# Optimization experiments

Measured on AMD Instinct MI355X. Metric: run time of the kernel, lower is better.

The kernel has to match this reference:

```python
import math
import jax, jax.numpy as jnp
import numpy as np

H = 256      # hidden_size
HEADS = 8
DK = H // HEADS
B = 32
DL = 290     # drug length
PL = 1000    # protein length


def _pe(length, d):
    # sinusoidal positional encoding, d even
    pos = jnp.arange(length, dtype=jnp.float32)[:, None]
    div = jnp.exp(jnp.arange(0, d, 2, dtype=jnp.float32) * (-math.log(10000.0) / d))
    ang = pos * div  # [L, d/2]
    pe = jnp.zeros((length, d), jnp.float32)
    pe = pe.at[:, 0::2].set(jnp.sin(ang)).at[:, 1::2].set(jnp.cos(ang))
    return pe


def setup_inputs() -> dict:
    key = jax.random.key(0)
    ks = iter(jax.random.split(key, 48))
    def lin(din, dout):
        return jax.random.normal(next(ks), (din, dout), jnp.float32) * 0.02, jnp.zeros((dout,), jnp.float32)
    inp = {}
    inp['drug'] = jax.random.normal(next(ks), (B, DL, H), jnp.float32)
    inp['protein'] = jax.random.normal(next(ks), (B, PL, H), jnp.float32)
    inp['scale_d'] = jnp.ones((1,), jnp.float32)
    inp['scale_p'] = jnp.ones((1,), jnp.float32)
    for name in ['q_d', 'k_p', 'v_p', 'q_p', 'k_d', 'v_d', 'out_d', 'out_p']:
        w, b = lin(H, H)
        inp['w_' + name] = w
        inp['b_' + name] = b
    inp['alpha'] = jnp.asarray(0.5, jnp.float32)
    for name in ['fc_dp', 'fc_pd']:
        w, b = lin(HEADS, H)
        inp['w_' + name] = w
        inp['b_' + name] = b
    for name in ['gd', 'gp']:
        w, b = lin(H, H)
        inp['w_' + name] = w
        inp['b_' + name] = b
    return inp


def _split_heads(x):
    b, l, _ = x.shape
    return x.reshape(b, l, HEADS, DK).transpose(0, 2, 1, 3)  # [b, h, l, dk]


def _forward(drug, protein, scale_d, scale_p,
             w_q_d, b_q_d, w_k_p, b_k_p, w_v_p, b_v_p,
             w_q_p, b_q_p, w_k_d, b_k_d, w_v_d, b_v_d,
             alpha, w_out_d, b_out_d, w_out_p, b_out_p,
             w_fc_dp, b_fc_dp, w_fc_pd, b_fc_pd,
             w_gd, b_gd, w_gp, b_gp):
    b, dl, h = drug.shape
    pl = protein.shape[1]
    # positional encoding (buffers, non-learned except scale)
    drug_e = drug + scale_d * _pe(dl, h)
    prot_e = protein + scale_p * _pe(pl, h)

    Qd = _split_heads(drug_e @ w_q_d + b_q_d)   # [b,h,dl,dk]
    Kp = _split_heads(prot_e @ w_k_p + b_k_p)   # [b,h,pl,dk]
    Vp = _split_heads(prot_e @ w_v_p + b_v_p)
    Qp = _split_heads(prot_e @ w_q_p + b_q_p)
    Kd = _split_heads(drug_e @ w_k_d + b_k_d)
    Vd = _split_heads(drug_e @ w_v_d + b_v_d)

    inv_sqrt = 1.0 / math.sqrt(DK)
    attn_dp = jnp.einsum('bhid,bhjd->bhij', Qd, Kp) * inv_sqrt      # [b,h,dl,pl]
    # (Q_p K_d^T)^T along last two dims -> [b,h,dl,pl]
    attn_pd = jnp.einsum('bhjd,bhid->bhij', Qp, Kd) * inv_sqrt
    a = jax.nn.sigmoid(alpha)
    A = jax.nn.softmax(a * attn_dp + (1.0 - a) * attn_pd, axis=-1)  # [b,h,dl,pl]

    ctx_d = jnp.einsum('bhij,bhjd->bhid', A, Vp)  # [b,h,dl,dk]
    ctx_p = jnp.einsum('bhij,bhid->bhjd', A, Vd)  # [b,h,pl,dk]
    ctx_d = ctx_d.transpose(0, 2, 1, 3).reshape(b, dl, h) @ w_out_d + b_out_d
    ctx_p = ctx_p.transpose(0, 2, 1, 3).reshape(b, pl, h) @ w_out_p + b_out_p

    attn_dp_m = jnp.mean(A, axis=-1).transpose(0, 2, 1)   # [b,dl,heads]
    drug_attn = attn_dp_m @ w_fc_dp + b_fc_dp             # [b,dl,h]
    attn_pd_m = jnp.mean(A, axis=-2).transpose(0, 2, 1)   # [b,pl,heads]
    prot_attn = attn_pd_m @ w_fc_pd + b_fc_pd             # [b,pl,h]

    drug_gate = jax.nn.sigmoid(drug_e @ w_gd + b_gd)
    prot_gate = jax.nn.sigmoid(prot_e @ w_gp + b_gp)
    ctx_d = ctx_d * drug_gate
    ctx_p = ctx_p * prot_gate

    drug_upd = drug_e + ctx_d * jax.nn.sigmoid(drug_attn)
    prot_upd = prot_e + ctx_p * jax.nn.sigmoid(prot_attn)
    return jnp.concatenate([drug_upd, prot_upd], axis=1)  # [b, dl+pl, h]


def reference(drug, protein, scale_d, scale_p,
              w_q_d, b_q_d, w_k_p, b_k_p, w_v_p, b_v_p,
              w_q_p, b_q_p, w_k_d, b_k_d, w_v_d, b_v_d,
              alpha, w_out_d, b_out_d, w_out_p, b_out_p,
              w_fc_dp, b_fc_dp, w_fc_pd, b_fc_pd,
              w_gd, b_gd, w_gp, b_gp):
    return _forward(drug, protein, scale_d, scale_p,
                    w_q_d, b_q_d, w_k_p, b_k_p, w_v_p, b_v_p,
                    w_q_p, b_q_p, w_k_d, b_k_d, w_v_d, b_v_d,
                    alpha, w_out_d, b_out_d, w_out_p, b_out_p,
                    w_fc_dp, b_fc_dp, w_fc_pd, b_fc_pd,
                    w_gd, b_gd, w_gp, b_gp)
```

## Files before the change

kernel.cpp:

```cpp
#include <hip/hip_runtime.h>
#include <math.h>

typedef __attribute__((ext_vector_type(8))) short bf16x8;
typedef __attribute__((ext_vector_type(4))) float f32x4;
typedef unsigned short u16;
typedef unsigned int u32;

#define DEVFN static __device__ __forceinline__

constexpr int NB  = 32;
constexpr int DLn = 290;
constexpr int PLc = 1000;
constexpr int MD  = NB * DLn;
constexpr int MP  = NB * PLc;
constexpr int NSTRIP = 645;
constexpr int SPLIT  = 145;
constexpr int SG     = 81;

DEVFN u16 f2b(float f) {
    u32 u = __builtin_bit_cast(u32, f);
    u32 r = u + 0x7fffu + ((u >> 16) & 1u);
    return (u16)(r >> 16);
}
DEVFN u16 f2bh(float f) { __bf16 h = (__bf16)f; return __builtin_bit_cast(u16, h); }
DEVFN float b2f(u16 s) { return __builtin_bit_cast(float, (u32)s << 16); }
DEVFN float sigm(float x) { return 1.0f / (1.0f + __expf(-x)); }
DEVFN float fexp2(float x) { return __builtin_amdgcn_exp2f(x); }
DEVFN int sw(int row, int col, int stride) { return row * stride + (col ^ ((row & 7) << 3)); }

__global__ void pe_kernel(float* __restrict__ pe) {
    int p = blockIdx.x, c = threadIdx.x;
    float div = __expf((float)(c & ~1) * (-9.210340371976184f / 256.0f));
    float ang = (float)p * div;
    pe[p * 256 + c] = (c & 1) ? cosf(ang) : sinf(ang);
}

__global__ void fcprep_kernel(const float* __restrict__ w, const float* __restrict__ b,
                              float* __restrict__ dfc) {
    int c = threadIdx.x;
    float s = b[c];
    #pragma unroll
    for (int hh = 0; hh < 8; hh++) s += 0.001f * w[hh * 256 + c];
    dfc[c] = s;
}

__global__ __launch_bounds__(256) void eadd_kernel(
        const float* __restrict__ drug, const float* __restrict__ prot,
        const float* __restrict__ scale_d, const float* __restrict__ scale_p,
        const float* __restrict__ pe,
        u16* __restrict__ e_d, u16* __restrict__ e_p) {
    int idx = blockIdx.x * 256 + threadIdx.x;
    int r = idx >> 6, c4 = (idx & 63) * 4;
    if (r < MD) {
        int i = r % DLn;
        float s = scale_d[0];
        float4 dv = *(const float4*)&drug[(size_t)r * 256 + c4];
        float4 pv = *(const float4*)&pe[i * 256 + c4];
        u16 o[4];
        o[0] = f2b(dv.x + s * pv.x); o[1] = f2b(dv.y + s * pv.y);
        o[2] = f2b(dv.z + s * pv.z); o[3] = f2b(dv.w + s * pv.w);
        *(uint2*)&e_d[(size_t)r * 256 + c4] = *(uint2*)o;
    } else {
        int rr = r - MD;
        int j = rr % PLc;
        float s = scale_p[0];
        float4 dv = *(const float4*)&prot[(size_t)rr * 256 + c4];
        float4 pv = *(const float4*)&pe[j * 256 + c4];
        u16 o[4];
        o[0] = f2b(dv.x + s * pv.x); o[1] = f2b(dv.y + s * pv.y);
        o[2] = f2b(dv.z + s * pv.z); o[3] = f2b(dv.w + s * pv.w);
        *(uint2*)&e_p[(size_t)rr * 256 + c4] = *(uint2*)o;
    }
}

struct WPtrs { const float* w[10]; };
__global__ __launch_bounds__(256) void wprep_kernel(WPtrs wp, u16* __restrict__ wt) {
    __shared__ u16 t[64][66];
    int m = blockIdx.y, tile = blockIdx.x;
    int k0 = (tile >> 2) * 64, n0 = (tile & 3) * 64;
    const float* w = wp.w[m];
    int r = threadIdx.x >> 6, c = threadIdx.x & 63;
    #pragma unroll
    for (int q = 0; q < 16; q++) {
        int rr = r + q * 4;
        t[rr][c] = f2b(w[(size_t)(k0 + rr) * 256 + n0 + c]);
    }
    __syncthreads();
    #pragma unroll
    for (int q = 0; q < 16; q++) {
        int rr = r + q * 4;
        wt[((size_t)m << 16) + (size_t)(n0 + rr) * 256 + k0 + c] = t[c][rr];
    }
}

struct PM { const u16* BT; const float* bias; u16* C; int sig; };
struct PCfg {
    const u16* Ab;
    PM m[4];
};
struct PCfg2 {
    PCfg c0, c1;
    const float* x0; const float* x1;
    const u16* gate0; const u16* gate1;
    const float* cm;
    const float* dfc;
    const float* wfc1; const float* bfc1;
    const float* scale0; const float* scale1;
    const float* pe;
    float* out;
};

template<int NM>
__global__ __launch_bounds__(256) void proj_kernel(PCfg2 cfgs) {
    const int d = blockIdx.x;
    const int x = d & 7, q = d >> 3;
    const int u  = (NM == 4) ? (q & 15) : (q & 3);
    const int sg = (NM == 4) ? (q >> 4) : (q >> 2);
    const int s = sg * 8 + x;
    if (s >= NSTRIP) return;
    const int mi = (NM == 4) ? (u >> 2) : 0;
    const int nt = (NM == 4) ? (u & 3) : u;
    const bool f1 = s < SPLIT;
    const int mt = f1 ? s : s - SPLIT;

    const u16* Ab   = f1 ? cfgs.c0.Ab : cfgs.c1.Ab;
    const u16*   BT   = f1 ? (mi==0?cfgs.c0.m[0].BT  :mi==1?cfgs.c0.m[1].BT  :mi==2?cfgs.c0.m[2].BT  :cfgs.c0.m[3].BT)
                           : (mi==0?cfgs.c1.m[0].BT  :mi==1?cfgs.c1.m[1].BT  :mi==2?cfgs.c1.m[2].BT  :cfgs.c1.m[3].BT);
    const float* bias = f1 ? (mi==0?cfgs.c0.m[0].bias:mi==1?cfgs.c0.m[1].bias:mi==2?cfgs.c0.m[2].bias:cfgs.c0.m[3].bias)
                           : (mi==0?cfgs.c1.m[0].bias:mi==1?cfgs.c1.m[1].bias:mi==2?cfgs.c1.m[2].bias:cfgs.c1.m[3].bias);
    u16*         C    = f1 ? (mi==0?cfgs.c0.m[0].C   :mi==1?cfgs.c0.m[1].C   :mi==2?cfgs.c0.m[2].C   :cfgs.c0.m[3].C)
                           : (mi==0?cfgs.c1.m[0].C   :mi==1?cfgs.c1.m[1].C   :mi==2?cfgs.c1.m[2].C   :cfgs.c1.m[3].C);
    const int    sig  = f1 ? (mi==0?cfgs.c0.m[0].sig :mi==1?cfgs.c0.m[1].sig :mi==2?cfgs.c0.m[2].sig :cfgs.c0.m[3].sig)
                           : (mi==0?cfgs.c1.m[0].sig :mi==1?cfgs.c1.m[1].sig :mi==2?cfgs.c1.m[2].sig :cfgs.c1.m[3].sig);

    __shared__ u16 Bs[64 * 256];
    __shared__ float fcb[(NM == 1) ? 2304 : 4];
    const int tid = threadIdx.x;
    const int lane = tid & 63, w = tid >> 6, ln = lane & 15, g = lane >> 4;

    const int gc = tid & 31;
    const int rb = (tid >> 5) * 8;
    uint4 bv[8];
    #pragma unroll
    for (int kk = 0; kk < 8; kk++) {
        const int r = rb + kk;
        const int nur = ((r >> 5) & 1) * 32 + ((r >> 2) & 3) * 8 + ((r >> 4) & 1) * 4 + (r & 3);
        bv[kk] = *(const uint4*)(BT + (size_t)(nt * 64 + nur) * 256 + gc * 8);
    }

    const int row = mt * 64 + w * 16 + ln;
    bf16x8 Af[8];
    {
        const u16* Ap = Ab + (size_t)row * 256 + g * 8;
        #pragma unroll
        for (int ks = 0; ks < 8; ks++)
            Af[ks] = *(const bf16x8*)(Ap + ks * 32);
    }

    if (NM == 1 && !f1) {
        *(float4*)&fcb[tid * 8]     = *(const float4*)&cfgs.wfc1[tid * 8];
        *(float4*)&fcb[tid * 8 + 4] = *(const float4*)&cfgs.wfc1[tid * 8 + 4];
        fcb[2048 + tid] = cfgs.bfc1[tid];
    }

    #pragma unroll
    for (int kk = 0; kk < 8; kk++) {
        const int r = rb + kk;
        *(uint4*)&Bs[sw(r, gc * 8, 256)] = bv[kk];
    }
    __syncthreads();

    f32x4 acc[4] = {};
    #pragma unroll
    for (int ks = 0; ks < 8; ks++) {
        #pragma unroll
        for (int ntl = 0; ntl < 4; ntl++) {
            bf16x8 bf = *(const bf16x8*)&Bs[sw(ntl * 16 + ln, ks * 32 + g * 8, 256)];
            acc[ntl] = __builtin_amdgcn_mfma_f32_16x16x32_bf16(bf, Af[ks], acc[ntl], 0, 0, 0);
        }
    }

    const int base0 = nt * 64 + g * 8, base1 = base0 + 32;
    f32x4 b0 = *(const f32x4*)&bias[base0];
    f32x4 b1 = *(const f32x4*)&bias[base0 + 4];
    f32x4 b2 = *(const f32x4*)&bias[base1];
    f32x4 b3 = *(const f32x4*)&bias[base1 + 4];
    float v[16];
    #pragma unroll
    for (int t = 0; t < 4; t++) {
        v[t]      = acc[0][t] + b0[t];
        v[4 + t]  = acc[1][t] + b1[t];
        v[8 + t]  = acc[2][t] + b2[t];
        v[12 + t] = acc[3][t] + b3[t];
    }
    if (NM == 4) {
        if (sig) {
            #pragma unroll
            for (int t = 0; t < 16; t++) v[t] = sigm(v[t]);
        }
        u16 o[16];
        #pragma unroll
        for (int t = 0; t < 16; t++) o[t] = f2b(v[t]);
        u16* Cp = C + (size_t)row * 256;
        *(uint4*)&Cp[base0] = *(uint4*)&o[0];
        *(uint4*)&Cp[base1] = *(uint4*)&o[8];
    } else {
        (void)C; (void)sig;
        const float* X     = f1 ? cfgs.x0 : cfgs.x1;
        const u16* gate    = f1 ? cfgs.gate0 : cfgs.gate1;
        const float* scale = f1 ? cfgs.scale0 : cfgs.scale1;
        const float* pe    = cfgs.pe;
        const float sc = scale[0];
        const int pos  = f1 ? (row % DLn) : (row % PLc);
        const int bidx = f1 ? (row / DLn) : (row / PLc);
        const int orow = bidx * 1290 + (f1 ? pos : 290 + pos);
        float aw[16];
        if (f1) {
            const float* dfc = cfgs.dfc;
            *(float4*)&aw[0]  = *(const float4*)&dfc[base0];
            *(float4*)&aw[4]  = *(const float4*)&dfc[base0 + 4];
            *(float4*)&aw[8]  = *(const float4*)&dfc[base1];
            *(float4*)&aw[12] = *(const float4*)&dfc[base1 + 4];
        } else {
            float cmv[8];
            float4 ca = *(const float4*)&cfgs.cm[(size_t)row * 8];
            float4 cb = *(const float4*)&cfgs.cm[(size_t)row * 8 + 4];
            cmv[0]=ca.x; cmv[1]=ca.y; cmv[2]=ca.z; cmv[3]=ca.w;
            cmv[4]=cb.x; cmv[5]=cb.y; cmv[6]=cb.z; cmv[7]=cb.w;
            #pragma unroll
            for (int t = 0; t < 16; t++) {
                const int col = (t < 8) ? (base0 + t) : (base1 + t - 8);
                float s2 = fcb[2048 + col];
                #pragma unroll
                for (int hh = 0; hh < 8; hh++) s2 += cmv[hh] * fcb[hh * 256 + col];
                aw[t] = s2;
            }
        }
        u16 ge[16];
        *(uint4*)&ge[0] = *(const uint4*)&gate[(size_t)row * 256 + base0];
        *(uint4*)&ge[8] = *(const uint4*)&gate[(size_t)row * 256 + base1];
        float outv[16];
        #pragma unroll
        for (int half = 0; half < 2; half++) {
            const int cb0 = half ? base1 : base0;
            #pragma unroll
            for (int t4 = 0; t4 < 2; t4++) {
                float4 xa = *(const float4*)&X[(size_t)row * 256 + cb0 + t4 * 4];
                float4 pa = *(const float4*)&pe[(size_t)pos * 256 + cb0 + t4 * 4];
                #pragma unroll
                for (int t = 0; t < 4; t++) {
                    const int idx = half * 8 + t4 * 4 + t;
                    float e = (&xa.x)[t] + sc * (&pa.x)[t];
                    outv[idx] = e + v[idx] * b2f(ge[idx]) * sigm(aw[idx]);
                }
            }
        }
        float* Op = cfgs.out + (size_t)orow * 256;
        *(float4*)&Op[base0]     = *(float4*)&outv[0];
        *(float4*)&Op[base0 + 4] = *(float4*)&outv[4];
        *(float4*)&Op[base1]     = *(float4*)&outv[8];
        *(float4*)&Op[base1 + 4] = *(float4*)&outv[12];
    }
}

__global__ __launch_bounds__(512) void attn_kernel(
        const u16* __restrict__ Qd, const u16* __restrict__ Kd, const u16* __restrict__ Vd,
        const u16* __restrict__ Kp, const u16* __restrict__ Vp, const u16* __restrict__ Qp,
        const float* __restrict__ alpha,
        u16* __restrict__ ctx_d, u16* __restrict__ ctx_p, float* __restrict__ cm) {
    __shared__ u16 Ks[2][64 * 64];
    __shared__ union {
        struct { u16 VpT[2][32 * 64]; u16 Pm[320 * 64]; } s1;
        struct { u16 PT[64 * 320]; u16 VdT[32 * 320]; } s2;
    } U;
    __shared__ float r_l[320];
    __shared__ float colpart[8][64];

    const int bh = blockIdx.x, b = bh >> 3, h = bh & 7;
    const int tid = threadIdx.x;
    const int w = tid >> 6, lane = tid & 63, ln = lane & 15, g = lane >> 4;

    const float a = sigm(alpha[0]);
    const float inv = 0.1767766952966369f;
    const float l2e = 1.4426950408889634f;
    const float sa = a * inv * l2e, sb = (1.0f - a) * inv * l2e;
    const int nmt = (w < 4) ? 3 : 2;
    const int mtsA[3] = { w, w + 8, w + 16 };

    const size_t rbd = (size_t)b * DLn * 256 + h * 32;
    const size_t rbp = (size_t)b * PLc * 256 + h * 32;

    bf16x8 Qf[3][2];
    #pragma unroll
    for (int t = 0; t < 3; t++) {
        const int i = mtsA[t] * 16 + ln;
        #pragma unroll
        for (int ks = 0; ks < 2; ks++) {
            u16 o[8] = {0,0,0,0,0,0,0,0};
            if (t < nmt && i < DLn) {
                const u16* src = (ks ? Kd : Qd) + rbd + (size_t)i * 256 + g * 8;
                const float s = ks ? sb : sa;
                uint4 v = *(const uint4*)src;
                u16 e[8]; *(uint4*)e = v;
                #pragma unroll
                for (int q = 0; q < 8; q++) o[q] = f2bh(b2f(e[q]) * s);
            }
            Qf[t][ks] = *(bf16x8*)o;
        }
    }

    const int s_jj = tid >> 3, s_ch = tid & 7;
    const u16* s_src = ((s_ch >> 2) ? Qp : Kp) + rbp + (s_ch & 3) * 8;
    const int v_j = tid & 63, v_d0 = (tid >> 6) * 4;

    {
        int j = s_jj;
        uint4 kv = (j < PLc) ? *(const uint4*)(s_src + (size_t)j * 256) : make_uint4(0,0,0,0);
        uint2 vv = (v_j < PLc) ? *(const uint2*)(Vp + rbp + (size_t)v_j * 256 + v_d0) : make_uint2(0,0);
        *(uint4*)&Ks[0][sw(s_jj, s_ch * 8, 64)] = kv;
        u16 e[4]; *(uint2*)e = vv;
        #pragma unroll
        for (int q = 0; q < 4; q++) U.s1.VpT[0][sw(v_d0 + q, v_j, 64)] = e[q];
    }
    __syncthreads();

    float rs[3] = {0.f, 0.f, 0.f};
    f32x4 accd[3][2] = {};
    for (int jt = 0; jt < 16; jt++) {
        const int cur = jt & 1, j0 = jt * 64;
        const int jn = j0 + 64 + s_jj;
        uint4 kv = (jn < PLc) ? *(const uint4*)(s_src + (size_t)jn * 256) : make_uint4(0,0,0,0);
        const int vn = j0 + 64 + v_j;
        uint2 vv = (vn < PLc) ? *(const uint2*)(Vp + rbp + (size_t)vn * 256 + v_d0) : make_uint2(0,0);

        bf16x8 kf[4][2];
        #pragma unroll
        for (int js = 0; js < 4; js++)
            #pragma unroll
            for (int ks = 0; ks < 2; ks++)
                kf[js][ks] = *(const bf16x8*)&Ks[cur][sw(js * 16 + ln, ks * 32 + g * 8, 64)];

        #pragma unroll
        for (int t = 0; t < 3; t++) {
            if (t >= nmt) break;
            const int mt = mtsA[t];
            f32x4 acc[4] = {};
            #pragma unroll
            for (int ks = 0; ks < 2; ks++)
                #pragma unroll
                for (int js = 0; js < 4; js++)
                    acc[js] = __builtin_amdgcn_mfma_f32_16x16x32_bf16(kf[js][ks], Qf[t][ks], acc[js], 0, 0, 0);
            const int irow = mt * 16 + ln;
            #pragma unroll
            for (int js = 0; js < 4; js++) {
                u16 pb[4];
                float psum = 0.f;
                #pragma unroll
                for (int r = 0; r < 4; r++) {
                    float p = fexp2(acc[js][r]);
                    psum += p;
                    pb[r] = f2bh(p);
                }
                rs[t] += psum;
                *(ushort4*)&U.s1.Pm[sw(irow, js * 16 + g * 4, 64)] = *(ushort4*)pb;
            }
        }
        #pragma unroll
        for (int t = 0; t < 3; t++) {
            if (t >= nmt) break;
            const int mt = mtsA[t];
            #pragma unroll
            for (int ks2 = 0; ks2 < 2; ks2++) {
                bf16x8 af = *(const bf16x8*)&U.s1.Pm[sw(mt * 16 + ln, ks2 * 32 + g * 8, 64)];
                #pragma unroll
                for (int nd = 0; nd < 2; nd++) {
                    bf16x8 bv = *(const bf16x8*)&U.s1.VpT[cur][sw(nd * 16 + ln, ks2 * 32 + g * 8, 64)];
                    accd[t][nd] = __builtin_amdgcn_mfma_f32_16x16x32_bf16(bv, af, accd[t][nd], 0, 0, 0);
                }
            }
        }
        *(uint4*)&Ks[cur ^ 1][sw(s_jj, s_ch * 8, 64)] = kv;
        {
            u16 e[4]; *(uint2*)e = vv;
            #pragma unroll
            for (int q = 0; q < 4; q++) U.s1.VpT[cur ^ 1][sw(v_d0 + q, v_j, 64)] = e[q];
        }
        __syncthreads();
    }

    #pragma unroll
    for (int t = 0; t < 3; t++) {
        float v = rs[t];
        v += __shfl_xor(v, 16);
        v += __shfl_xor(v, 32);
        rs[t] = v;
    }
    if (g == 0) {
        #pragma unroll
        for (int t = 0; t < 3; t++) {
            if (t >= nmt) break;
            const int i = mtsA[t] * 16 + ln;
            r_l[i] = (i < DLn) ? 1.0f / (rs[t] - 24.0f) : 0.0f;
        }
    }
    __syncthreads();

    #pragma unroll
    for (int t = 0; t < 3; t++) {
        if (t >= nmt) break;
        const int i = mtsA[t] * 16 + ln;
        if (i < DLn) {
            const float ri = r_l[i];
            #pragma unroll
            for (int nd = 0; nd < 2; nd++) {
                u16 o[4];
                #pragma unroll
                for (int r = 0; r < 4; r++) o[r] = f2bh(accd[t][nd][r] * ri);
                *(uint2*)&ctx_d[rbd + (size_t)i * 256 + nd * 16 + g * 4] = *(uint2*)o;
            }
        }
    }
    for (int c = tid; c < 320 * 8; c += 512) {
        const int i = c >> 3, d0 = (c & 7) * 4;
        u16 o[4] = {0,0,0,0};
        if (i < DLn) {
            const float ri = r_l[i];
            uint2 v = *(const uint2*)(Vd + rbd + (size_t)i * 256 + d0);
            u16 e[4]; *(uint2*)e = v;
            #pragma unroll
            for (int q = 0; q < 4; q++) o[q] = f2bh(b2f(e[q]) * ri);
        }
        #pragma unroll
        for (int q = 0; q < 4; q++) U.s2.VdT[sw(d0 + q, i, 320)] = o[q];
    }
    {
        int j = s_jj;
        uint4 kv = (j < PLc) ? *(const uint4*)(s_src + (size_t)j * 256) : make_uint4(0,0,0,0);
        *(uint4*)&Ks[0][sw(s_jj, s_ch * 8, 64)] = kv;
    }
    float rr[3][4];
    #pragma unroll
    for (int t = 0; t < 3; t++)
        #pragma unroll
        for (int r = 0; r < 4; r++)
            rr[t][r] = (t < nmt) ? r_l[mtsA[t] * 16 + g * 4 + r] : 0.0f;
    __syncthreads();

    for (int jt = 0; jt < 16; jt++) {
        const int cur = jt & 1, j0 = jt * 64;
        const int jn = j0 + 64 + s_jj;
        uint4 kv = (jn < PLc) ? *(const uint4*)(s_src + (size_t)jn * 256) : make_uint4(0,0,0,0);

        bf16x8 kf[4][2];
        #pragma unroll
        for (int js = 0; js < 4; js++)
            #pragma unroll
            for (int ks = 0; ks < 2; ks++)
                kf[js][ks] = *(const bf16x8*)&Ks[cur][sw(js * 16 + ln, ks * 32 + g * 8, 64)];

        float csl[4] = {0.f, 0.f, 0.f, 0.f};
        #pragma unroll
        for (int t = 0; t < 3; t++) {
            if (t >= nmt) break;
            const int mt = mtsA[t];
            f32x4 acc[4] = {};
            #pragma unroll
            for (int ks = 0; ks < 2; ks++)
                #pragma unroll
                for (int js = 0; js < 4; js++)
                    acc[js] = __builtin_amdgcn_mfma_f32_16x16x32_bf16(Qf[t][ks], kf[js][ks], acc[js], 0, 0, 0);
            #pragma unroll
            for (int js = 0; js < 4; js++) {
                u16 pb[4];
                #pragma unroll
                for (int r = 0; r < 4; r++) {
                    float p = fexp2(acc[js][r]);
                    csl[js] += p * rr[t][r];
                    pb[r] = f2bh(p);
                }
                *(ushort4*)&U.s2.PT[sw(js * 16 + ln, mt * 16 + g * 4, 320)] = *(ushort4*)pb;
            }
        }
        #pragma unroll
        for (int js = 0; js < 4; js++) {
            float v = csl[js];
            v += __shfl_xor(v, 16);
            v += __shfl_xor(v, 32);
            csl[js] = v;
        }
        if (g == 0) {
            #pragma unroll
            for (int js = 0; js < 4; js++) colpart[w][js * 16 + ln] = csl[js];
        }
        *(uint4*)&Ks[cur ^ 1][sw(s_jj, s_ch * 8, 64)] = kv;
        __syncthreads();

        {
            const int js2 = w & 3, ds2 = w >> 2;
            f32x4 ap = {};
            #pragma unroll
            for (int k = 0; k < 10; k++) {
                bf16x8 af = *(const bf16x8*)&U.s2.PT[sw(js2 * 16 + ln, k * 32 + g * 8, 320)];
                bf16x8 bv = *(const bf16x8*)&U.s2.VdT[sw(ds2 * 16 + ln, k * 32 + g * 8, 320)];
                ap = __builtin_amdgcn_mfma_f32_16x16x32_bf16(bv, af, ap, 0, 0, 0);
            }
            const int j = j0 + js2 * 16 + ln;
            if (j < PLc) {
                u16 o[4];
                #pragma unroll
                for (int r = 0; r < 4; r++) o[r] = f2bh(ap[r]);
                *(uint2*)&ctx_p[rbp + (size_t)j * 256 + ds2 * 16 + g * 4] = *(uint2*)o;
            }
        }
        if (w == 0) {
            float tot = 0.f;
            #pragma unroll
            for (int ww = 0; ww < 8; ww++) tot += colpart[ww][lane];
            const int j = j0 + lane;
            if (j < PLc) cm[(size_t)(b * PLc + j) * 8 + h] = tot * (1.0f / 290.0f);
        }
        __syncthreads();
    }
}

extern "C" void kernel_launch(void* const* d_in, const int* in_sizes, int n_in,
                              void* d_out, int out_size, void* d_ws, size_t ws_size,
                              hipStream_t stream) {
    (void)in_sizes; (void)n_in; (void)out_size;
    const float* drug    = (const float*)d_in[0];
    const float* prot    = (const float*)d_in[1];
    const float* scale_d = (const float*)d_in[2];
    const float* scale_p = (const float*)d_in[3];

    char* ws = (char*)d_ws;
    size_t off = 0;
    auto alloc = [&](size_t bytes) -> void* {
        void* p = ws + off;
        off += (bytes + 255) & ~(size_t)255;
        return p;
    };
    float* pe   = (float*)alloc((size_t)1000 * 256 * 4);
    u16* wt     = (u16*)alloc((size_t)10 * 65536 * 2);
    u16* e_d    = (u16*)alloc((size_t)MD * 256 * 2);
    u16* e_p    = (u16*)alloc((size_t)MP * 256 * 2);
    u16* Qd     = (u16*)alloc((size_t)MD * 256 * 2);
    u16* Kd     = (u16*)alloc((size_t)MD * 256 * 2);
    u16* Vd     = (u16*)alloc((size_t)MD * 256 * 2);
    u16* gate_d = (u16*)alloc((size_t)MD * 256 * 2);
    u16* Kp     = (u16*)alloc((size_t)MP * 256 * 2);
    u16* Vp     = (u16*)alloc((size_t)MP * 256 * 2);
    u16* Qp     = (u16*)alloc((size_t)MP * 256 * 2);
    u16* gate_p = (u16*)alloc((size_t)MP * 256 * 2);
    u16* ctxd   = (u16*)alloc((size_t)MD * 256 * 2);
    u16* ctxp   = (u16*)alloc((size_t)MP * 256 * 2);
    float* cm   = (float*)alloc((size_t)MP * 8 * 4);
    float* dfc  = (float*)alloc((size_t)256 * 4);
    if (off > ws_size) return;

    pe_kernel<<<1000, 256, 0, stream>>>(pe);
    fcprep_kernel<<<1, 256, 0, stream>>>((const float*)d_in[21], (const float*)d_in[22], dfc);

    WPtrs wp;
    const int wsrc[10] = {4, 12, 14, 25, 6, 8, 10, 27, 16, 18};
    for (int m = 0; m < 10; m++) wp.w[m] = (const float*)d_in[wsrc[m]];
    wprep_kernel<<<dim3(16, 10), 256, 0, stream>>>(wp, wt);

    eadd_kernel<<<(MD + MP) / 4, 256, 0, stream>>>(drug, prot, scale_d, scale_p, pe, e_d, e_p);

    auto W = [&](int slot) { return wt + (size_t)slot * 65536; };

    PCfg2 p1 = {};
    p1.c0 = { e_d,
              { { W(0), (const float*)d_in[5],  Qd,     0 },
                { W(1), (const float*)d_in[13], Kd,     0 },
                { W(2), (const float*)d_in[15], Vd,     0 },
                { W(3), (const float*)d_in[26], gate_d, 1 } } };
    p1.c1 = { e_p,
              { { W(4), (const float*)d_in[7],  Kp,     0 },
                { W(5), (const float*)d_in[9],  Vp,     0 },
                { W(6), (const float*)d_in[11], Qp,     0 },
                { W(7), (const float*)d_in[28], gate_p, 1 } } };
    proj_kernel<4><<<SG * 8 * 16, 256, 0, stream>>>(p1);

    attn_kernel<<<256, 512, 0, stream>>>(Qd, Kd, Vd, Kp, Vp, Qp,
                                         (const float*)d_in[20], ctxd, ctxp, cm);

    PCfg2 p2 = {};
    p2.c0 = { ctxd, { { W(8), (const float*)d_in[17], nullptr, 0 }, {}, {}, {} } };
    p2.c1 = { ctxp, { { W(9), (const float*)d_in[19], nullptr, 0 }, {}, {}, {} } };
    p2.x0 = drug;  p2.x1 = prot;
    p2.gate0 = gate_d;  p2.gate1 = gate_p;
    p2.cm = cm;
    p2.dfc = dfc;
    p2.wfc1 = (const float*)d_in[23];  p2.bfc1 = (const float*)d_in[24];
    p2.scale0 = scale_d;  p2.scale1 = scale_p;
    p2.pe = pe;
    p2.out = (float*)d_out;
    proj_kernel<1><<<SG * 8 * 4, 256, 0, stream>>>(p2);
}
```

Measured before the change: 175.3 us.

## Split attention over drug-row halves to double block count, merge partials downstream

The attention kernel now runs two blocks per (batch, head), each handling half of the drug rows (160 padded). Each half writes its own partial protein-side context and column-mean buffers, and the output projection kernel sums the two partials on load. This doubles the grid from 256 to 512 blocks to fill more compute units and shrinks per-block LDS. The cost is that the protein-side K/V streaming is done twice, extra workspace is written and read, and the partial contexts are rounded to bf16 before they are summed.

```diff
diff --git a/kernel.cpp b/kernel.cpp
--- a/kernel.cpp
+++ b/kernel.cpp
@@ -16,6 +16,8 @@
 constexpr int NSTRIP = 645;
 constexpr int SPLIT  = 145;
 constexpr int SG     = 81;
+constexpr int IRH    = 160;
+constexpr int PSTR   = 192;
 
 DEVFN u16 f2b(float f) {
     u32 u = __builtin_bit_cast(u32, f);
@@ -100,9 +102,10 @@
 };
 struct PCfg2 {
     PCfg c0, c1;
+    const u16* abp1;
     const float* x0; const float* x1;
     const u16* gate0; const u16* gate1;
-    const float* cm;
+    const float* cm; const float* cmB;
     const float* dfc;
     const float* wfc1; const float* bfc1;
     const float* scale0; const float* scale1;
@@ -150,7 +153,20 @@
 
     const int row = mt * 64 + w * 16 + ln;
     bf16x8 Af[8];
-    {
+    if (NM == 1 && !f1) {
+        const u16* Ap0 = Ab + (size_t)row * 256 + g * 8;
+        const u16* Ap1 = cfgs.abp1 + (size_t)row * 256 + g * 8;
+        #pragma unroll
+        for (int ks = 0; ks < 8; ks++) {
+            uint4 v0 = *(const uint4*)(Ap0 + ks * 32);
+            uint4 v1 = *(const uint4*)(Ap1 + ks * 32);
+            u16 e0[8], e1[8], o[8];
+            *(uint4*)e0 = v0; *(uint4*)e1 = v1;
+            #pragma unroll
+            for (int qq = 0; qq < 8; qq++) o[qq] = f2bh(b2f(e0[qq]) + b2f(e1[qq]));
+            Af[ks] = *(bf16x8*)o;
+        }
+    } else {
         const u16* Ap = Ab + (size_t)row * 256 + g * 8;
         #pragma unroll
         for (int ks = 0; ks < 8; ks++)
@@ -225,8 +241,10 @@
             float cmv[8];
             float4 ca = *(const float4*)&cfgs.cm[(size_t)row * 8];
             float4 cb = *(const float4*)&cfgs.cm[(size_t)row * 8 + 4];
-            cmv[0]=ca.x; cmv[1]=ca.y; cmv[2]=ca.z; cmv[3]=ca.w;
-            cmv[4]=cb.x; cmv[5]=cb.y; cmv[6]=cb.z; cmv[7]=cb.w;
+            float4 da_ = *(const float4*)&cfgs.cmB[(size_t)row * 8];
+            float4 db_ = *(const float4*)&cfgs.cmB[(size_t)row * 8 + 4];
+            cmv[0]=ca.x+da_.x; cmv[1]=ca.y+da_.y; cmv[2]=ca.z+da_.z; cmv[3]=ca.w+da_.w;
+            cmv[4]=cb.x+db_.x; cmv[5]=cb.y+db_.y; cmv[6]=cb.z+db_.z; cmv[7]=cb.w+db_.w;
             #pragma unroll
             for (int t = 0; t < 16; t++) {
                 const int col = (t < 8) ? (base0 + t) : (base1 + t - 8);
@@ -267,16 +285,21 @@
         const u16* __restrict__ Qd, const u16* __restrict__ Kd, const u16* __restrict__ Vd,
         const u16* __restrict__ Kp, const u16* __restrict__ Vp, const u16* __restrict__ Qp,
         const float* __restrict__ alpha,
-        u16* __restrict__ ctx_d, u16* __restrict__ ctx_p, float* __restrict__ cm) {
+        u16* __restrict__ ctx_d, u16* __restrict__ ctxp0, u16* __restrict__ ctxp1,
+        float* __restrict__ cm0, float* __restrict__ cm1) {
     __shared__ u16 Ks[2][64 * 64];
     __shared__ union {
-        struct { u16 VpT[2][32 * 64]; u16 Pm[320 * 64]; } s1;
-        struct { u16 PT[64 * 320]; u16 VdT[32 * 320]; } s2;
+        struct { u16 VpT[2][32 * 64]; u16 Pm[IRH * 64]; } s1;
+        struct { u16 PT[64 * PSTR]; u16 VdT[32 * PSTR]; } s2;
     } U;
-    __shared__ float r_l[320];
+    __shared__ float r_l[IRH];
     __shared__ float colpart[8][64];
 
-    const int bh = blockIdx.x, b = bh >> 3, h = bh & 7;
+    const int blk = blockIdx.x, bh = blk >> 1, half = blk & 1;
+    const int b = bh >> 3, h = bh & 7;
+    const int i0 = half * IRH;
+    u16* ctx_p = half ? ctxp1 : ctxp0;
+    float* cm  = half ? cm1 : cm0;
     const int tid = threadIdx.x;
     const int w = tid >> 6, lane = tid & 63, ln = lane & 15, g = lane >> 4;
 
@@ -284,26 +307,26 @@
     const float inv = 0.1767766952966369f;
     const float l2e = 1.4426950408889634f;
     const float sa = a * inv * l2e, sb = (1.0f - a) * inv * l2e;
-    const int nmt = (w < 4) ? 3 : 2;
-    const int mtsA[3] = { w, w + 8, w + 16 };
+    const int nmt = (w < 2) ? 2 : 1;
+    const int mtsA[2] = { w, w + 8 };
 
     const size_t rbd = (size_t)b * DLn * 256 + h * 32;
     const size_t rbp = (size_t)b * PLc * 256 + h * 32;
 
-    bf16x8 Qf[3][2];
-    #pragma unroll
-    for (int t = 0; t < 3; t++) {
-        const int i = mtsA[t] * 16 + ln;
+    bf16x8 Qf[2][2];
+    #pragma unroll
+    for (int t = 0; t < 2; t++) {
+        const int ig = i0 + mtsA[t] * 16 + ln;
         #pragma unroll
         for (int ks = 0; ks < 2; ks++) {
             u16 o[8] = {0,0,0,0,0,0,0,0};
-            if (t < nmt && i < DLn) {
-                const u16* src = (ks ? Kd : Qd) + rbd + (size_t)i * 256 + g * 8;
+            if (t < nmt && ig < DLn) {
+                const u16* src = (ks ? Kd : Qd) + rbd + (size_t)ig * 256 + g * 8;
                 const float s = ks ? sb : sa;
                 uint4 v = *(const uint4*)src;
                 u16 e[8]; *(uint4*)e = v;
                 #pragma unroll
-                for (int q = 0; q < 8; q++) o[q] = f2bh(b2f(e[q]) * s);
+                for (int qq = 0; qq < 8; qq++) o[qq] = f2bh(b2f(e[qq]) * s);
             }
             Qf[t][ks] = *(bf16x8*)o;
         }
@@ -320,12 +343,12 @@
         *(uint4*)&Ks[0][sw(s_jj, s_ch * 8, 64)] = kv;
         u16 e[4]; *(uint2*)e = vv;
         #pragma unroll
-        for (int q = 0; q < 4; q++) U.s1.VpT[0][sw(v_d0 + q, v_j, 64)] = e[q];
+        for (int qq = 0; qq < 4; qq++) U.s1.VpT[0][sw(v_d0 + qq, v_j, 64)] = e[qq];
     }
     __syncthreads();
 
-    float rs[3] = {0.f, 0.f, 0.f};
-    f32x4 accd[3][2] = {};
+    float rs[2] = {0.f, 0.f};
+    f32x4 accd[2][2] = {};
     for (int jt = 0; jt < 16; jt++) {
         const int cur = jt & 1, j0 = jt * 64;
         const int jn = j0 + 64 + s_jj;
@@ -341,7 +364,7 @@
                 kf[js][ks] = *(const bf16x8*)&Ks[cur][sw(js * 16 + ln, ks * 32 + g * 8, 64)];
 
         #pragma unroll
-        for (int t = 0; t < 3; t++) {
+        for (int t = 0; t < 2; t++) {
             if (t >= nmt) break;
             const int mt = mtsA[t];
             f32x4 acc[4] = {};
@@ -366,7 +389,7 @@
             }
         }
         #pragma unroll
-        for (int t = 0; t < 3; t++) {
+        for (int t = 0; t < 2; t++) {
             if (t >= nmt) break;
             const int mt = mtsA[t];
             #pragma unroll
@@ -374,8 +397,8 @@
                 bf16x8 af = *(const bf16x8*)&U.s1.Pm[sw(mt * 16 + ln, ks2 * 32 + g * 8, 64)];
                 #pragma unroll
                 for (int nd = 0; nd < 2; nd++) {
-                    bf16x8 bv = *(const bf16x8*)&U.s1.VpT[cur][sw(nd * 16 + ln, ks2 * 32 + g * 8, 64)];
-                    accd[t][nd] = __builtin_amdgcn_mfma_f32_16x16x32_bf16(bv, af, accd[t][nd], 0, 0, 0);
+                    bf16x8 bvv = *(const bf16x8*)&U.s1.VpT[cur][sw(nd * 16 + ln, ks2 * 32 + g * 8, 64)];
+                    accd[t][nd] = __builtin_amdgcn_mfma_f32_16x16x32_bf16(bvv, af, accd[t][nd], 0, 0, 0);
                 }
             }
         }
@@ -383,13 +406,13 @@
         {
             u16 e[4]; *(uint2*)e = vv;
             #pragma unroll
-            for (int q = 0; q < 4; q++) U.s1.VpT[cur ^ 1][sw(v_d0 + q, v_j, 64)] = e[q];
+            for (int qq = 0; qq < 4; qq++) U.s1.VpT[cur ^ 1][sw(v_d0 + qq, v_j, 64)] = e[qq];
         }
         __syncthreads();
     }
 
     #pragma unroll
-    for (int t = 0; t < 3; t++) {
+    for (int t = 0; t < 2; t++) {
         float v = rs[t];
         v += __shfl_xor(v, 16);
         v += __shfl_xor(v, 32);
@@ -397,50 +420,52 @@
     }
     if (g == 0) {
         #pragma unroll
-        for (int t = 0; t < 3; t++) {
+        for (int t = 0; t < 2; t++) {
             if (t >= nmt) break;
-            const int i = mtsA[t] * 16 + ln;
-            r_l[i] = (i < DLn) ? 1.0f / (rs[t] - 24.0f) : 0.0f;
+            const int il = mtsA[t] * 16 + ln;
+            r_l[il] = (i0 + il < DLn) ? 1.0f / (rs[t] - 24.0f) : 0.0f;
         }
     }
     __syncthreads();
 
     #pragma unroll
-    for (int t = 0; t < 3; t++) {
+    for (int t = 0; t < 2; t++) {
         if (t >= nmt) break;
-        const int i = mtsA[t] * 16 + ln;
-        if (i < DLn) {
-            const float ri = r_l[i];
+        const int il = mtsA[t] * 16 + ln;
+        const int ig = i0 + il;
+        if (ig < DLn) {
+            const float ri = r_l[il];
             #pragma unroll
             for (int nd = 0; nd < 2; nd++) {
                 u16 o[4];
                 #pragma unroll
                 for (int r = 0; r < 4; r++) o[r] = f2bh(accd[t][nd][r] * ri);
-                *(uint2*)&ctx_d[rbd + (size_t)i * 256 + nd * 16 + g * 4] = *(uint2*)o;
-            }
-        }
-    }
-    for (int c = tid; c < 320 * 8; c += 512) {
-        const int i = c >> 3, d0 = (c & 7) * 4;
+                *(uint2*)&ctx_d[rbd + (size_t)ig * 256 + nd * 16 + g * 4] = *(uint2*)o;
+            }
+        }
+    }
+    for (int c = tid; c < IRH * 8; c += 512) {
+        const int il = c >> 3, d0 = (c & 7) * 4;
+        const int ig = i0 + il;
         u16 o[4] = {0,0,0,0};
-        if (i < DLn) {
-            const float ri = r_l[i];
-            uint2 v = *(const uint2*)(Vd + rbd + (size_t)i * 256 + d0);
+        if (ig < DLn) {
+            const float ri = r_l[il];
+            uint2 v = *(const uint2*)(Vd + rbd + (size_t)ig * 256 + d0);
             u16 e[4]; *(uint2*)e = v;
             #pragma unroll
-            for (int q = 0; q < 4; q++) o[q] = f2bh(b2f(e[q]) * ri);
-        }
-        #pragma unroll
-        for (int q = 0; q < 4; q++) U.s2.VdT[sw(d0 + q, i, 320)] = o[q];
+            for (int qq = 0; qq < 4; qq++) o[qq] = f2bh(b2f(e[qq]) * ri);
+        }
+        #pragma unroll
+        for (int qq = 0; qq < 4; qq++) U.s2.VdT[sw(d0 + qq, il, PSTR)] = o[qq];
     }
     {
         int j = s_jj;
         uint4 kv = (j < PLc) ? *(const uint4*)(s_src + (size_t)j * 256) : make_uint4(0,0,0,0);
         *(uint4*)&Ks[0][sw(s_jj, s_ch * 8, 64)] = kv;
     }
-    float rr[3][4];
-    #pragma unroll
-    for (int t = 0; t < 3; t++)
+    float rr[2][4];
+    #pragma unroll
+    for (int t = 0; t < 2; t++)
         #pragma unroll
         for (int r = 0; r < 4; r++)
             rr[t][r] = (t < nmt) ? r_l[mtsA[t] * 16 + g * 4 + r] : 0.0f;
@@ -460,7 +485,7 @@
 
         float csl[4] = {0.f, 0.f, 0.f, 0.f};
         #pragma unroll
-        for (int t = 0; t < 3; t++) {
+        for (int t = 0; t < 2; t++) {
             if (t >= nmt) break;
             const int mt = mtsA[t];
             f32x4 acc[4] = {};
@@ -478,7 +503,7 @@
                     csl[js] += p * rr[t][r];
                     pb[r] = f2bh(p);
                 }
-                *(ushort4*)&U.s2.PT[sw(js * 16 + ln, mt * 16 + g * 4, 320)] = *(ushort4*)pb;
+                *(ushort4*)&U.s2.PT[sw(js * 16 + ln, mt * 16 + g * 4, PSTR)] = *(ushort4*)pb;
             }
         }
         #pragma unroll
@@ -499,10 +524,10 @@
             const int js2 = w & 3, ds2 = w >> 2;
             f32x4 ap = {};
             #pragma unroll
-            for (int k = 0; k < 10; k++) {
-                bf16x8 af = *(const bf16x8*)&U.s2.PT[sw(js2 * 16 + ln, k * 32 + g * 8, 320)];
-                bf16x8 bv = *(const bf16x8*)&U.s2.VdT[sw(ds2 * 16 + ln, k * 32 + g * 8, 320)];
-                ap = __builtin_amdgcn_mfma_f32_16x16x32_bf16(bv, af, ap, 0, 0, 0);
+            for (int k = 0; k < IRH / 32; k++) {
+                bf16x8 af = *(const bf16x8*)&U.s2.PT[sw(js2 * 16 + ln, k * 32 + g * 8, PSTR)];
+                bf16x8 bvv = *(const bf16x8*)&U.s2.VdT[sw(ds2 * 16 + ln, k * 32 + g * 8, PSTR)];
+                ap = __builtin_amdgcn_mfma_f32_16x16x32_bf16(bvv, af, ap, 0, 0, 0);
             }
             const int j = j0 + js2 * 16 + ln;
             if (j < PLc) {
@@ -552,8 +577,10 @@
     u16* Qp     = (u16*)alloc((size_t)MP * 256 * 2);
     u16* gate_p = (u16*)alloc((size_t)MP * 256 * 2);
     u16* ctxd   = (u16*)alloc((size_t)MD * 256 * 2);
-    u16* ctxp   = (u16*)alloc((size_t)MP * 256 * 2);
-    float* cm   = (float*)alloc((size_t)MP * 8 * 4);
+    u16* ctxp0  = (u16*)alloc((size_t)MP * 256 * 2);
+    u16* ctxp1  = (u16*)alloc((size_t)MP * 256 * 2);
+    float* cm0  = (float*)alloc((size_t)MP * 8 * 4);
+    float* cm1  = (float*)alloc((size_t)MP * 8 * 4);
     float* dfc  = (float*)alloc((size_t)256 * 4);
     if (off > ws_size) return;
 
@@ -582,15 +609,16 @@
                 { W(7), (const float*)d_in[28], gate_p, 1 } } };
     proj_kernel<4><<<SG * 8 * 16, 256, 0, stream>>>(p1);
 
-    attn_kernel<<<256, 512, 0, stream>>>(Qd, Kd, Vd, Kp, Vp, Qp,
-                                         (const float*)d_in[20], ctxd, ctxp, cm);
+    attn_kernel<<<512, 512, 0, stream>>>(Qd, Kd, Vd, Kp, Vp, Qp,
+                                         (const float*)d_in[20], ctxd, ctxp0, ctxp1, cm0, cm1);
 
     PCfg2 p2 = {};
-    p2.c0 = { ctxd, { { W(8), (const float*)d_in[17], nullptr, 0 }, {}, {}, {} } };
-    p2.c1 = { ctxp, { { W(9), (const float*)d_in[19], nullptr, 0 }, {}, {}, {} } };
+    p2.c0 = { ctxd,  { { W(8), (const float*)d_in[17], nullptr, 0 }, {}, {}, {} } };
+    p2.c1 = { ctxp0, { { W(9), (const float*)d_in[19], nullptr, 0 }, {}, {}, {} } };
+    p2.abp1 = ctxp1;
     p2.x0 = drug;  p2.x1 = prot;
     p2.gate0 = gate_d;  p2.gate1 = gate_p;
-    p2.cm = cm;
+    p2.cm = cm0;  p2.cmB = cm1;
     p2.dfc = dfc;
     p2.wfc1 = (const float*)d_in[23];  p2.bfc1 = (const float*)d_in[24];
     p2.scale0 = scale_d;  p2.scale1 = scale_p;
```

Result: slower. 206.2 us (+17.7%).
